# Performance work log

Measured on AMD Instinct MI355X. Metric: run time of the kernel, lower is better.

## Reference

```python
import jax, jax.numpy as jnp
import numpy as np
from jax import lax


def _dwconv1d(x, w, b):
    # x: (B, C, S); w: (C, 1, k) torch-style depthwise weight; pad (k-1)//2
    k = w.shape[-1]
    p = (k - 1) // 2
    y = lax.conv_general_dilated(
        x, w, window_strides=(1,), padding=[(p, p)],
        dimension_numbers=("NCH", "OIH", "NCH"),
        feature_group_count=x.shape[1])
    return y + b[None, :, None]


def setup_inputs() -> dict:
    key = jax.random.key(0)
    ks = jax.random.split(key, 8)
    B, S, D = 4, 8192, 768
    W = 3 * D
    s = 0.02
    return {
        "x": jax.random.normal(ks[0], (B, S, D), jnp.float32),
        "w_in": jax.random.normal(ks[1], (W, D), jnp.float32) * s,
        "b_in": jnp.zeros((W,), jnp.float32),
        "w_short": jax.random.normal(ks[2], (W, 1, 3), jnp.float32) * s,
        "b_short": jnp.zeros((W,), jnp.float32),
        "w_cond1": jax.random.normal(ks[3], (D, 1, 3), jnp.float32) * s,
        "b_cond1": jnp.zeros((D,), jnp.float32),
        "w_cond2": jax.random.normal(ks[4], (D, 1, 3), jnp.float32) * s,
        "b_cond2": jnp.zeros((D,), jnp.float32),
        "h0": jax.random.normal(ks[5], (1, S, D), jnp.float32) * s,
        "w_out": jax.random.normal(ks[6], (D, D), jnp.float32) * s,
        "b_out": jnp.zeros((D,), jnp.float32),
    }


def reference(x, w_in, b_in, w_short, b_short, w_cond1, b_cond1,
              w_cond2, b_cond2, h0, w_out, b_out):
    D = h0.shape[-1]
    # in projection: (B,S,3D)
    x3 = jnp.einsum("bsd,ed->bse", x, w_in) + b_in
    v = x3[..., 2 * D:]                       # (B,S,D)
    # conditioning branch: depthwise conv -> |rfft| -> depthwise conv
    v_t = jnp.swapaxes(v, 1, 2)               # (B,D,S)
    hc = _dwconv1d(v_t, w_cond1, b_cond1)     # (B,D,S)
    hmag = jnp.abs(jnp.fft.rfft(hc, axis=2))  # (B,D,E), E=S//2+1
    h_adapt_f = _dwconv1d(hmag, w_cond2, b_cond2)  # (B,D,E) real
    # short depthwise filter over all 3D channels
    x_t = jnp.swapaxes(x3, 1, 2)              # (B,3D,S)
    x_t = _dwconv1d(x_t, w_short, b_short)
    s1, s2, vv = jnp.split(x_t, 3, axis=1)    # each (B,D,S)
    y = vv * s1
    # adaptive long convolution in frequency domain
    h0_t = jnp.swapaxes(h0, 1, 2)             # (1,D,S)
    h0_f = jnp.fft.rfft(h0_t, axis=-1)        # (1,D,E) complex
    x_f = jnp.fft.rfft(y, axis=-1)            # (B,D,E) complex
    y = jnp.fft.irfft(x_f * (h0_f + h_adapt_f), axis=-1)  # (B,D,S)
    y = y * s2
    y = jnp.swapaxes(y, 1, 2)                 # (B,S,D)
    out = jnp.einsum("bsd,ed->bse", y, w_out) + b_out
    return out
```

## Files before the change

### kernel.cpp

```cpp
#include <hip/hip_runtime.h>
#include <math.h>


typedef unsigned short u16;
typedef short s16x8 __attribute__((ext_vector_type(8)));
typedef float f32x4 __attribute__((ext_vector_type(4)));
typedef u16 u16x8 __attribute__((ext_vector_type(8)));

#define LPZ(i) ((i) ^ (((i) >> 4) & 15) ^ (((i) >> 8) & 15))
#define BREV13(k) ((int)(__brev((unsigned)(k)) >> 19))
#define BREV12(k) ((int)(__brev((unsigned)(k)) >> 20))
#define CMUL(rr, ri, xr, xi, wr, wi) { rr = (xr)*(wr) - (xi)*(wi); ri = (xr)*(wi) + (xi)*(wr); }

__device__ __forceinline__ u16 f2bf(float f) {
  unsigned u = __float_as_uint(f);
  u = (u + 0x7FFFu + ((u >> 16) & 1u)) >> 16;
  return (u16)u;
}
__device__ __forceinline__ float bf2f(u16 u) { return __uint_as_float(((unsigned)u) << 16); }

__device__ __forceinline__ void glds16(const void* g, void* l) {
  __builtin_amdgcn_global_load_lds((const __attribute__((address_space(1))) unsigned*)g,
                                   (__attribute__((address_space(3))) unsigned*)l, 16, 0, 0);
}

__global__ __launch_bounds__(256) void cvt_bf16(const float* __restrict__ in,
                                                u16* __restrict__ out, int n8) {
  const int i = blockIdx.x * 256 + threadIdx.x;
  if (i < n8) {
    const float4 a = ((const float4*)in)[i * 2];
    const float4 b = ((const float4*)in)[i * 2 + 1];
    u16x8 r;
    r[0] = f2bf(a.x); r[1] = f2bf(a.y); r[2] = f2bf(a.z); r[3] = f2bf(a.w);
    r[4] = f2bf(b.x); r[5] = f2bf(b.y); r[6] = f2bf(b.z); r[7] = f2bf(b.w);
    ((u16x8*)out)[i] = r;
  }
}

template <int BIAS_M>
__global__ __launch_bounds__(256) void gemm_bt(const u16* __restrict__ A,
                                               const u16* __restrict__ B,
                                               const float* __restrict__ bias,
                                               void* __restrict__ Cout,
                                               int N, int K,
                                               size_t As_str, size_t Cs_str) {
  __shared__ __align__(16) u16 As[4096];
  __shared__ __align__(16) u16 Bs[4096];
  A += (size_t)blockIdx.z * As_str;
  const int tid = threadIdx.x;
  const int w = tid >> 6, l = tid & 63;
  const int m0 = blockIdx.y * 128, n0 = blockIdx.x * 128;
  const int wr = w >> 1, wc = w & 1;
  const int lr = l & 15, kc = l >> 4;

  const int p0 = w * 64 + l;
  const int p1 = p0 + 256;
  const int sl0 = (p0 & 7) ^ ((p0 >> 3) & 7);
  const int sl1 = (p1 & 7) ^ ((p1 >> 3) & 7);
  const int r0 = ((p0 >> 3) << 1) | (sl0 >> 2), ka = (sl0 & 3) << 3;
  const int r1 = ((p1 >> 3) << 1) | (sl1 >> 2), kb = (sl1 & 3) << 3;
  const u16* gA0 = A + (size_t)(m0 + r0) * K + ka;
  const u16* gA1 = A + (size_t)(m0 + r1) * K + kb;
  const u16* gB0 = B + (size_t)(n0 + r0) * K + ka;
  const u16* gB1 = B + (size_t)(n0 + r1) * K + kb;
  u16* lA0 = &As[(size_t)w * 512];
  u16* lA1 = &As[(size_t)(4 + w) * 512];
  u16* lB0 = &Bs[(size_t)w * 512];
  u16* lB1 = &Bs[(size_t)(4 + w) * 512];

  f32x4 acc[4][4] = {};

  for (int k0 = 0; k0 < K; k0 += 32) {
    glds16(gA0 + k0, lA0);
    glds16(gA1 + k0, lA1);
    glds16(gB0 + k0, lB0);
    glds16(gB1 + k0, lB1);
    __syncthreads();
    s16x8 af[4], bfr[4];
#pragma unroll
    for (int mi = 0; mi < 4; ++mi) {
      const int row = wr * 64 + mi * 16 + lr;
      const int slot = (((lr & 1) << 2) | kc) ^ ((lr >> 1) & 7);
      af[mi] = *(const s16x8*)&As[(row >> 1) * 64 + slot * 8];
    }
#pragma unroll
    for (int ni = 0; ni < 4; ++ni) {
      const int row = wc * 64 + ni * 16 + lr;
      const int slot = (((lr & 1) << 2) | kc) ^ ((lr >> 1) & 7);
      bfr[ni] = *(const s16x8*)&Bs[(row >> 1) * 64 + slot * 8];
    }
#pragma unroll
    for (int mi = 0; mi < 4; ++mi)
#pragma unroll
      for (int ni = 0; ni < 4; ++ni)
        acc[mi][ni] = __builtin_amdgcn_mfma_f32_16x16x32_bf16(af[mi], bfr[ni], acc[mi][ni], 0, 0, 0);
    __syncthreads();
  }

  const int rbase = m0 + wr * 64 + (kc << 2);
  const int cbase = n0 + wc * 64 + lr;
#pragma unroll
  for (int mi = 0; mi < 4; ++mi)
#pragma unroll
    for (int j = 0; j < 4; ++j) {
      const int row = rbase + mi * 16 + j;
      const float bm = BIAS_M ? bias[row] : 0.f;
#pragma unroll
      for (int ni = 0; ni < 4; ++ni) {
        const int col = cbase + ni * 16;
        const float v = acc[mi][ni][j] + (BIAS_M ? bm : bias[col]);
        if (BIAS_M) ((u16*)Cout)[(size_t)row * N + col] = f2bf(v);
        else ((float*)Cout)[(size_t)blockIdx.z * Cs_str + (size_t)row * N + col] = v;
      }
    }
}

__global__ void twfill(float2* __restrict__ tw) {
  const int k = blockIdx.x * 256 + threadIdx.x;
  if (k < 8192) {
    const double t = -2.0 * 3.14159265358979323846 * (double)k / 8192.0;
    tw[k] = make_float2((float)cos(t), (float)sin(t));
  }
}

__global__ __launch_bounds__(256) void transp(const float* __restrict__ in, float* __restrict__ out) {
  __shared__ float T[64][65];
  const int d0 = blockIdx.x * 64, s0 = blockIdx.y * 64;
  const int c = threadIdx.x & 63, r0 = threadIdx.x >> 6;
#pragma unroll
  for (int i = 0; i < 16; ++i) {
    const int r = r0 + i * 4;
    T[r][c] = in[(size_t)(s0 + r) * 768 + d0 + c];
  }
  __syncthreads();
#pragma unroll
  for (int i = 0; i < 16; ++i) {
    const int r = r0 + i * 4;
    out[(size_t)(d0 + r) * 8192 + s0 + c] = T[c][r];
  }
}

__device__ __forceinline__ void dif4(float2& A, float2& B, float2& C, float2& D,
                                     float2 w1, float2 w2, float2 w3) {
  const float apr = A.x + C.x, api = A.y + C.y, amr = A.x - C.x, ami = A.y - C.y;
  const float bpr = B.x + D.x, bpi = B.y + D.y, bmr = B.x - D.x, bmi = B.y - D.y;
  const float2 o0 = make_float2(apr + bpr, api + bpi);
  const float x1r = apr - bpr, x1i = api - bpi;
  float2 o1; CMUL(o1.x, o1.y, x1r, x1i, w2.x, w2.y);
  const float x2r = amr + bmi, x2i = ami - bmr;
  float2 o2; CMUL(o2.x, o2.y, x2r, x2i, w1.x, w1.y);
  const float x3r = amr - bmi, x3i = ami + bmr;
  float2 o3; CMUL(o3.x, o3.y, x3r, x3i, w3.x, w3.y);
  A = o0; B = o1; C = o2; D = o3;
}

__device__ __forceinline__ void dit4(float2& A, float2& B, float2& C, float2& D,
                                     float2 w1, float2 w2) {
  float vbr, vbi, vdr, vdi;
  CMUL(vbr, vbi, B.x, B.y, w2.x, w2.y);
  CMUL(vdr, vdi, D.x, D.y, w2.x, w2.y);
  const float a1r = A.x + vbr, a1i = A.y + vbi;
  const float b1r = A.x - vbr, b1i = A.y - vbi;
  const float c1r = C.x + vdr, c1i = C.y + vdi;
  const float d1r = C.x - vdr, d1i = C.y - vdi;
  float t1r, t1i, ur, ui;
  CMUL(t1r, t1i, c1r, c1i, w1.x, w1.y);
  CMUL(ur, ui, d1r, d1i, w1.y, -w1.x);
  A = make_float2(a1r + t1r, a1i + t1i);
  C = make_float2(a1r - t1r, a1i - t1i);
  B = make_float2(b1r + ur,  b1i + ui);
  D = make_float2(b1r - ur,  b1i - ui);
}

__device__ __forceinline__ void fwd_pass16(float2* z, const float2* __restrict__ tw,
                                           int base, int jp, int st, int e) {
  float2 v[16]; int idx[16];
#pragma unroll
  for (int m = 0; m < 16; ++m) { idx[m] = LPZ(base + m * st); v[m] = z[idx[m]]; }
#pragma unroll
  for (int c = 0; c < 4; ++c) {
    const int jc = jp + c * st;
    dif4(v[c], v[c + 4], v[c + 8], v[c + 12],
         tw[jc << e], tw[(2 * jc) << e], tw[(3 * jc) << e]);
  }
  const float2 u1 = tw[jp << (e + 2)];
  const float2 u2 = tw[(2 * jp) << (e + 2)];
  const float2 u3 = tw[(3 * jp) << (e + 2)];
#pragma unroll
  for (int a = 0; a < 4; ++a)
    dif4(v[4 * a], v[4 * a + 1], v[4 * a + 2], v[4 * a + 3], u1, u2, u3);
#pragma unroll
  for (int m = 0; m < 16; ++m) z[idx[m]] = v[m];
}

__device__ __forceinline__ void inv_pass16(float2* z, const float2* __restrict__ tw,
                                           int base, int jp, int st, int e) {
  float2 v[16]; int idx[16];
#pragma unroll
  for (int m = 0; m < 16; ++m) { idx[m] = LPZ(base + m * st); v[m] = z[idx[m]]; }
  const float2 w1 = tw[jp << e];
  const float2 w2 = tw[(2 * jp) << e];
#pragma unroll
  for (int a = 0; a < 4; ++a)
    dit4(v[4 * a], v[4 * a + 1], v[4 * a + 2], v[4 * a + 3], w1, w2);
#pragma unroll
  for (int c = 0; c < 4; ++c) {
    const int jpp = c * st + jp;
    dit4(v[c], v[c + 4], v[c + 8], v[c + 12],
         tw[jpp << (e - 2)], tw[(2 * jpp) << (e - 2)]);
  }
#pragma unroll
  for (int m = 0; m < 16; ++m) z[idx[m]] = v[m];
}

template <int NT>
__device__ __forceinline__ void fwd8192(float2* z, const float2* __restrict__ tw, int tid) {
  fwd_pass16(z, tw, tid, tid, 512, 0);
  __syncthreads();
  fwd_pass16(z, tw, ((tid >> 5) << 9) | (tid & 31), tid & 31, 32, 4);
  __syncthreads();
  fwd_pass16(z, tw, ((tid >> 1) << 5) | (tid & 1), tid & 1, 2, 8);
  __syncthreads();
#pragma unroll
  for (int t = 0; t < 8; ++t) {
    const int g = tid + t * 512;
    const int p = LPZ(2 * g), q = LPZ(2 * g + 1);
    const float2 U = z[p], V = z[q];
    z[p] = make_float2(U.x + V.x, U.y + V.y);
    z[q] = make_float2(U.x - V.x, U.y - V.y);
  }
  __syncthreads();
}

template <int NT>
__device__ __forceinline__ void inv4096(float2* z, const float2* __restrict__ tw, int tid) {
  if (tid < 256) inv_pass16(z, tw, tid << 4, 0, 1, 11);
  __syncthreads();
  if (tid < 256) inv_pass16(z, tw, ((tid >> 4) << 8) | (tid & 15), tid & 15, 16, 7);
  __syncthreads();
  if (tid < 256) inv_pass16(z, tw, tid, tid, 256, 3);
  __syncthreads();
}

__global__ __launch_bounds__(512, 2) void fft_h0_k(const float* __restrict__ h0T,
                                                   const float2* __restrict__ tw,
                                                   float2* __restrict__ h0f) {
  __shared__ float2 z[8192];
  const int d = blockIdx.x, tid = threadIdx.x;
  const float* src = h0T + (size_t)d * 8192;
  const int s0 = tid << 4;
#pragma unroll
  for (int m = 0; m < 16; ++m) z[LPZ(s0 + m)] = make_float2(src[s0 + m], 0.f);
  __syncthreads();
  fwd8192<512>(z, tw, tid);
  for (int k = tid; k <= 4096; k += 512) {
    h0f[(size_t)d * 4097 + k] = z[LPZ(BREV13(k))];
  }
}

__global__ __launch_bounds__(512, 2) void fused_fft(u16* __restrict__ x3T,
                                                    const float2* __restrict__ tw,
                                                    const float2* __restrict__ h0f,
                                                    const float* __restrict__ w_short,
                                                    const float* __restrict__ b_short,
                                                    const float* __restrict__ w_cond1,
                                                    const float* __restrict__ b_cond1,
                                                    const float* __restrict__ w_cond2,
                                                    const float* __restrict__ b_cond2,
                                                    size_t bstr) {
  __shared__ float2 z[8192];
  const int d = blockIdx.x, tid = threadIdx.x;
  x3T += (size_t)blockIdx.y * bstr;
  u16* g0 = x3T + (size_t)d * 8192;
  const u16* g1 = x3T + (size_t)(768 + d) * 8192;
  const u16* g2 = x3T + (size_t)(1536 + d) * 8192;

  const float q0 = w_cond1[d * 3], q1 = w_cond1[d * 3 + 1], q2 = w_cond1[d * 3 + 2], bc1 = b_cond1[d];
  const float t00 = w_short[d * 3], t01 = w_short[d * 3 + 1], t02 = w_short[d * 3 + 2], bs0 = b_short[d];
  const float t10 = w_short[(768 + d) * 3], t11 = w_short[(768 + d) * 3 + 1], t12 = w_short[(768 + d) * 3 + 2], bs1 = b_short[768 + d];
  const float t20 = w_short[(1536 + d) * 3], t21 = w_short[(1536 + d) * 3 + 1], t22 = w_short[(1536 + d) * 3 + 2], bs2 = b_short[1536 + d];

  const int s0 = tid << 4;

  {
    const u16x8 ga0 = *(const u16x8*)&g0[s0];
    const u16x8 ga1 = *(const u16x8*)&g0[s0 + 8];
    const u16x8 gb0 = *(const u16x8*)&g2[s0];
    const u16x8 gb1 = *(const u16x8*)&g2[s0 + 8];
    float a[18], bz[18];
    a[0]  = s0 ? bf2f(g0[s0 - 1]) : 0.f;
    bz[0] = s0 ? bf2f(g2[s0 - 1]) : 0.f;
#pragma unroll
    for (int m = 0; m < 8; ++m) {
      a[1 + m] = bf2f(ga0[m]);  a[9 + m] = bf2f(ga1[m]);
      bz[1 + m] = bf2f(gb0[m]); bz[9 + m] = bf2f(gb1[m]);
    }
    a[17]  = (s0 + 16 < 8192) ? bf2f(g0[s0 + 16]) : 0.f;
    bz[17] = (s0 + 16 < 8192) ? bf2f(g2[s0 + 16]) : 0.f;
#pragma unroll
    for (int m = 0; m < 16; ++m) {
      const float s1v = t00 * a[m] + t01 * a[m + 1] + t02 * a[m + 2] + bs0;
      const float vvv = t20 * bz[m] + t21 * bz[m + 1] + t22 * bz[m + 2] + bs2;
      const float hcv = q0 * bz[m] + q1 * bz[m + 1] + q2 * bz[m + 2] + bc1;
      z[LPZ(s0 + m)] = make_float2(hcv, s1v * vvv);
    }
  }
  __syncthreads();

  fwd8192<512>(z, tw, tid);

  float hm[9], yr[9], yi[9];
#pragma unroll
  for (int j = 0; j < 9; ++j) {
    const int k = tid + j * 512;
    if (k <= 4096) {
      const float2 Zk = z[LPZ(BREV13(k))];
      const float2 Zm = z[LPZ(BREV13((8192 - k) & 8191))];
      const float hcr = 0.5f * (Zk.x + Zm.x), hci = 0.5f * (Zk.y - Zm.y);
      hm[j] = sqrtf(hcr * hcr + hci * hci);
      yr[j] = 0.5f * (Zk.y + Zm.y);
      yi[j] = 0.5f * (Zm.x - Zk.x);
    }
  }
  __syncthreads();
  float* hbuf = (float*)z;
#pragma unroll
  for (int j = 0; j < 9; ++j) { const int k = tid + j * 512; if (k <= 4096) hbuf[k] = hm[j]; }
  __syncthreads();

  const float c0 = w_cond2[d * 3], c1 = w_cond2[d * 3 + 1], c2 = w_cond2[d * 3 + 2], bb2 = b_cond2[d];
  const float2* H0 = h0f + (size_t)d * 4097;
  float gr[9], gi[9];
#pragma unroll
  for (int j = 0; j < 9; ++j) {
    const int k = tid + j * 512;
    if (k <= 4096) {
      const float a = k ? hbuf[k - 1] : 0.f;
      const float m = hbuf[k];
      const float zn = (k < 4096) ? hbuf[k + 1] : 0.f;
      const float ha = c0 * a + c1 * m + c2 * zn + bb2;
      const float2 h = H0[k];
      const float hr = h.x + ha, hi = h.y;
      gr[j] = yr[j] * hr - yi[j] * hi;
      gi[j] = yr[j] * hi + yi[j] * hr;
      if (k == 0 || k == 4096) gi[j] = 0.f;
    }
  }
  __syncthreads();
#pragma unroll
  for (int j = 0; j < 9; ++j) {
    const int k = tid + j * 512;
    if (k <= 4096) z[LPZ(k)] = make_float2(gr[j], gi[j]);
  }
  __syncthreads();

  float zr2[8], zi2[8];
#pragma unroll
  for (int j = 0; j < 8; ++j) {
    const int kc = tid + j * 512;
    const float2 Ga = z[LPZ(kc)];
    const float2 Gb = z[LPZ(4096 - kc)];
    const float Er = 0.5f * (Ga.x + Gb.x), Ei = 0.5f * (Ga.y - Gb.y);
    const float Pr = 0.5f * (Ga.x - Gb.x), Pi = 0.5f * (Ga.y + Gb.y);
    const float2 w = tw[kc];
    const float Or = Pr * w.x + Pi * w.y;
    const float Oi = Pi * w.x - Pr * w.y;
    zr2[j] = Er - Oi;
    zi2[j] = -(Ei + Or);
  }
  __syncthreads();
#pragma unroll
  for (int j = 0; j < 8; ++j) {
    const int kc = tid + j * 512;
    z[LPZ(BREV12(kc))] = make_float2(zr2[j], zi2[j]);
  }
  __syncthreads();

  inv4096<512>(z, tw, tid);

  {
    const u16x8 g1a = *(const u16x8*)&g1[s0];
    const u16x8 g1b = *(const u16x8*)&g1[s0 + 8];
    float gg[18];
    gg[0] = s0 ? bf2f(g1[s0 - 1]) : 0.f;
#pragma unroll
    for (int m = 0; m < 8; ++m) { gg[1 + m] = bf2f(g1a[m]); gg[9 + m] = bf2f(g1b[m]); }
    gg[17] = (s0 + 16 < 8192) ? bf2f(g1[s0 + 16]) : 0.f;
    float2 zv[8];
#pragma unroll
    for (int r = 0; r < 8; ++r) zv[r] = z[LPZ((s0 >> 1) + r)];
    const float invM = 1.0f / 4096.0f;
    u16x8 o0, o1;
#pragma unroll
    for (int m = 0; m < 16; ++m) {
      const float xs = ((m & 1) ? -zv[m >> 1].y : zv[m >> 1].x) * invM;
      const float s2v = t10 * gg[m] + t11 * gg[m + 1] + t12 * gg[m + 2] + bs1;
      const u16 val = f2bf(xs * s2v);
      if (m < 8) o0[m] = val; else o1[m - 8] = val;
    }
    *(u16x8*)&g0[s0] = o0;
    *(u16x8*)&g0[s0 + 8] = o1;
  }
}

__global__ __launch_bounds__(256) void y2t(const u16* __restrict__ y2rows, u16* __restrict__ y2b,
                                           size_t in_str, size_t out_str) {
  __shared__ u16 T[64][65];
  y2rows += (size_t)blockIdx.z * in_str;
  y2b    += (size_t)blockIdx.z * out_str;
  const int d0 = blockIdx.x * 64, s0 = blockIdx.y * 64;
  const int c = threadIdx.x & 63, r0 = threadIdx.x >> 6;
#pragma unroll
  for (int i = 0; i < 16; ++i) {
    const int r = r0 + i * 4;
    T[r][c] = y2rows[(size_t)(d0 + r) * 8192 + s0 + c];
  }
  __syncthreads();
#pragma unroll
  for (int i = 0; i < 16; ++i) {
    const int r = r0 + i * 4;
    y2b[(size_t)(s0 + r) * 768 + d0 + c] = T[c][r];
  }
}

extern "C" void kernel_launch(void* const* d_in, const int* in_sizes, int n_in,
                              void* d_out, int out_size, void* d_ws, size_t ws_size,
                              hipStream_t stream) {
  (void)in_sizes; (void)n_in; (void)out_size;
  const float* x       = (const float*)d_in[0];
  const float* w_in    = (const float*)d_in[1];
  const float* b_in    = (const float*)d_in[2];
  const float* w_short = (const float*)d_in[3];
  const float* b_short = (const float*)d_in[4];
  const float* w_cond1 = (const float*)d_in[5];
  const float* b_cond1 = (const float*)d_in[6];
  const float* w_cond2 = (const float*)d_in[7];
  const float* b_cond2 = (const float*)d_in[8];
  const float* h0      = (const float*)d_in[9];
  const float* w_out   = (const float*)d_in[10];
  const float* b_out   = (const float*)d_in[11];

  float* ws = (float*)d_ws;
  float2* tw     = (float2*)ws;
  float2* h0f    = (float2*)(ws + 16384);
  u16*    xb     = (u16*)(ws + 6309376);
  u16*    w_inb  = (u16*)(ws + 9455104);
  u16*    w_outb = (u16*)(ws + 10339840);
  u16*    x3Tb   = (u16*)(ws + 10634752);
  float*  h0T    = (float*)(ws + 6309376);

  const size_t BSTR = 18874368ull;
  const bool merged = ws_size >= 193533952ull;

  twfill<<<32, 256, 0, stream>>>(tw);
  transp<<<dim3(12, 128), 256, 0, stream>>>(h0, h0T);
  fft_h0_k<<<768, 512, 0, stream>>>(h0T, tw, h0f);
  cvt_bf16<<<864, 256, 0, stream>>>(w_in, w_inb, 221184);
  cvt_bf16<<<288, 256, 0, stream>>>(w_out, w_outb, 73728);

  if (merged) {
    for (int b = 0; b < 4; ++b) {
      cvt_bf16<<<3072, 256, 0, stream>>>(x + (size_t)b * 6291456, xb, 786432);
      gemm_bt<1><<<dim3(64, 18), 256, 0, stream>>>(w_inb, xb, b_in,
                                                   x3Tb + (size_t)b * BSTR, 8192, 768, 0, 0);
    }
    fused_fft<<<dim3(768, 4), 512, 0, stream>>>(x3Tb, tw, h0f,
                                                w_short, b_short, w_cond1, b_cond1,
                                                w_cond2, b_cond2, BSTR);
    y2t<<<dim3(12, 128, 4), 256, 0, stream>>>(x3Tb, x3Tb + 6291456, BSTR, BSTR);
    gemm_bt<0><<<dim3(6, 64, 4), 256, 0, stream>>>(x3Tb + 6291456, w_outb, b_out,
                                                   (float*)d_out, 768, 768,
                                                   BSTR, 6291456ull);
  } else {
    for (int b = 0; b < 4; ++b) {
      cvt_bf16<<<3072, 256, 0, stream>>>(x + (size_t)b * 6291456, xb, 786432);
      gemm_bt<1><<<dim3(64, 18), 256, 0, stream>>>(w_inb, xb, b_in, x3Tb, 8192, 768, 0, 0);
      fused_fft<<<dim3(768, 1), 512, 0, stream>>>(x3Tb, tw, h0f,
                                                  w_short, b_short, w_cond1, b_cond1,
                                                  w_cond2, b_cond2, 0);
      y2t<<<dim3(12, 128, 1), 256, 0, stream>>>(x3Tb, x3Tb + 6291456, 0, 0);
      gemm_bt<0><<<dim3(6, 64, 1), 256, 0, stream>>>(x3Tb + 6291456, w_outb, b_out,
                                                     (float*)d_out + (size_t)b * 6291456,
                                                     768, 768, 0, 0);
    }
  }
}
```

Baseline: 579.4 us.

## Batch input GEMM over all batches and pair h0 FFTs via complex packing

Adds a workspace tier that converts all of x to bf16 at once and runs the input projection GEMM as a single batched launch over the z grid dimension, instead of four serial convert+GEMM launches. The GEMM gains a B-operand batch stride and a batched output stride for the bf16 path. The h0 filter FFT now packs two real channels into one complex transform and separates them with conjugate symmetry, halving the number of FFT blocks. The new batched path needs a larger workspace, and it only runs when the workspace passes that larger size threshold.

```diff
diff --git a/kernel.cpp b/kernel.cpp
--- a/kernel.cpp
+++ b/kernel.cpp
@@ -43,10 +43,11 @@
                                                const float* __restrict__ bias,
                                                void* __restrict__ Cout,
                                                int N, int K,
-                                               size_t As_str, size_t Cs_str) {
+                                               size_t As_str, size_t Bs_str, size_t Cs_str) {
   __shared__ __align__(16) u16 As[4096];
   __shared__ __align__(16) u16 Bs[4096];
   A += (size_t)blockIdx.z * As_str;
+  B += (size_t)blockIdx.z * Bs_str;
   const int tid = threadIdx.x;
   const int w = tid >> 6, l = tid & 63;
   const int m0 = blockIdx.y * 128, n0 = blockIdx.x * 128;
@@ -109,7 +110,7 @@
       for (int ni = 0; ni < 4; ++ni) {
         const int col = cbase + ni * 16;
         const float v = acc[mi][ni][j] + (BIAS_M ? bm : bias[col]);
-        if (BIAS_M) ((u16*)Cout)[(size_t)row * N + col] = f2bf(v);
+        if (BIAS_M) ((u16*)Cout)[(size_t)blockIdx.z * Cs_str + (size_t)row * N + col] = f2bf(v);
         else ((float*)Cout)[(size_t)blockIdx.z * Cs_str + (size_t)row * N + col] = v;
       }
     }
@@ -242,19 +243,25 @@
   __syncthreads();
 }
 
-__global__ __launch_bounds__(512, 2) void fft_h0_k(const float* __restrict__ h0T,
-                                                   const float2* __restrict__ tw,
-                                                   float2* __restrict__ h0f) {
+__global__ __launch_bounds__(512, 2) void fft_h0_pair(const float* __restrict__ h0T,
+                                                      const float2* __restrict__ tw,
+                                                      float2* __restrict__ h0f) {
   __shared__ float2 z[8192];
-  const int d = blockIdx.x, tid = threadIdx.x;
-  const float* src = h0T + (size_t)d * 8192;
+  const int d0 = blockIdx.x * 2, tid = threadIdx.x;
+  const float* srcA = h0T + (size_t)d0 * 8192;
+  const float* srcB = srcA + 8192;
   const int s0 = tid << 4;
 #pragma unroll
-  for (int m = 0; m < 16; ++m) z[LPZ(s0 + m)] = make_float2(src[s0 + m], 0.f);
+  for (int m = 0; m < 16; ++m) z[LPZ(s0 + m)] = make_float2(srcA[s0 + m], srcB[s0 + m]);
   __syncthreads();
   fwd8192<512>(z, tw, tid);
+  float2* H0 = h0f + (size_t)d0 * 4097;
+  float2* H1 = H0 + 4097;
   for (int k = tid; k <= 4096; k += 512) {
-    h0f[(size_t)d * 4097 + k] = z[LPZ(BREV13(k))];
+    const float2 Zk = z[LPZ(BREV13(k))];
+    const float2 Zm = z[LPZ(BREV13((8192 - k) & 8191))];
+    H0[k] = make_float2(0.5f * (Zk.x + Zm.x), 0.5f * (Zk.y - Zm.y));
+    H1[k] = make_float2(0.5f * (Zk.y + Zm.y), 0.5f * (Zm.x - Zk.x));
   }
 }
 
@@ -441,47 +448,72 @@
   const float* b_out   = (const float*)d_in[11];
 
   float* ws = (float*)d_ws;
-  float2* tw     = (float2*)ws;
-  float2* h0f    = (float2*)(ws + 16384);
-  u16*    xb     = (u16*)(ws + 6309376);
-  u16*    w_inb  = (u16*)(ws + 9455104);
-  u16*    w_outb = (u16*)(ws + 10339840);
-  u16*    x3Tb   = (u16*)(ws + 10634752);
-  float*  h0T    = (float*)(ws + 6309376);
-
+  float2* tw  = (float2*)ws;
+  float2* h0f = (float2*)(ws + 16384);
+  float*  h0T = ws + 6309376;
   const size_t BSTR = 18874368ull;
-  const bool merged = ws_size >= 193533952ull;
+  const size_t XSTR = 6291456ull;
+
+  const bool t1 = ws_size >= 231282688ull;
+  const bool t2 = !t1 && ws_size >= 193533952ull;
 
   twfill<<<32, 256, 0, stream>>>(tw);
   transp<<<dim3(12, 128), 256, 0, stream>>>(h0, h0T);
-  fft_h0_k<<<768, 512, 0, stream>>>(h0T, tw, h0f);
-  cvt_bf16<<<864, 256, 0, stream>>>(w_in, w_inb, 221184);
-  cvt_bf16<<<288, 256, 0, stream>>>(w_out, w_outb, 73728);
-
-  if (merged) {
+  fft_h0_pair<<<384, 512, 0, stream>>>(h0T, tw, h0f);
+
+  if (t1) {
+    u16* xb4    = (u16*)(ws + 6309376);
+    u16* w_inb  = (u16*)(ws + 18892288);
+    u16* w_outb = (u16*)(ws + 19777024);
+    u16* x3Tb4  = (u16*)(ws + 20071936);
+    cvt_bf16<<<864, 256, 0, stream>>>(w_in, w_inb, 221184);
+    cvt_bf16<<<288, 256, 0, stream>>>(w_out, w_outb, 73728);
+    cvt_bf16<<<12288, 256, 0, stream>>>(x, xb4, 3145728);
+    gemm_bt<1><<<dim3(64, 18, 4), 256, 0, stream>>>(w_inb, xb4, b_in, x3Tb4,
+                                                    8192, 768, 0, XSTR, BSTR);
+    fused_fft<<<dim3(768, 4), 512, 0, stream>>>(x3Tb4, tw, h0f,
+                                                w_short, b_short, w_cond1, b_cond1,
+                                                w_cond2, b_cond2, BSTR);
+    y2t<<<dim3(12, 128, 4), 256, 0, stream>>>(x3Tb4, x3Tb4 + XSTR, BSTR, BSTR);
+    gemm_bt<0><<<dim3(6, 64, 4), 256, 0, stream>>>(x3Tb4 + XSTR, w_outb, b_out,
+                                                   (float*)d_out, 768, 768,
+                                                   BSTR, 0, XSTR);
+  } else if (t2) {
+    u16* xb     = (u16*)(ws + 6309376);
+    u16* w_inb  = (u16*)(ws + 9455104);
+    u16* w_outb = (u16*)(ws + 10339840);
+    u16* x3Tb   = (u16*)(ws + 10634752);
+    cvt_bf16<<<864, 256, 0, stream>>>(w_in, w_inb, 221184);
+    cvt_bf16<<<288, 256, 0, stream>>>(w_out, w_outb, 73728);
     for (int b = 0; b < 4; ++b) {
-      cvt_bf16<<<3072, 256, 0, stream>>>(x + (size_t)b * 6291456, xb, 786432);
+      cvt_bf16<<<3072, 256, 0, stream>>>(x + (size_t)b * XSTR, xb, 786432);
       gemm_bt<1><<<dim3(64, 18), 256, 0, stream>>>(w_inb, xb, b_in,
-                                                   x3Tb + (size_t)b * BSTR, 8192, 768, 0, 0);
+                                                   x3Tb + (size_t)b * BSTR, 8192, 768, 0, 0, 0);
     }
     fused_fft<<<dim3(768, 4), 512, 0, stream>>>(x3Tb, tw, h0f,
                                                 w_short, b_short, w_cond1, b_cond1,
                                                 w_cond2, b_cond2, BSTR);
-    y2t<<<dim3(12, 128, 4), 256, 0, stream>>>(x3Tb, x3Tb + 6291456, BSTR, BSTR);
-    gemm_bt<0><<<dim3(6, 64, 4), 256, 0, stream>>>(x3Tb + 6291456, w_outb, b_out,
+    y2t<<<dim3(12, 128, 4), 256, 0, stream>>>(x3Tb, x3Tb + XSTR, BSTR, BSTR);
+    gemm_bt<0><<<dim3(6, 64, 4), 256, 0, stream>>>(x3Tb + XSTR, w_outb, b_out,
                                                    (float*)d_out, 768, 768,
-                                                   BSTR, 6291456ull);
+                                                   BSTR, 0, XSTR);
   } else {
+    u16* xb     = (u16*)(ws + 6309376);
+    u16* w_inb  = (u16*)(ws + 9455104);
+    u16* w_outb = (u16*)(ws + 10339840);
+    u16* x3Tb   = (u16*)(ws + 10634752);
+    cvt_bf16<<<864, 256, 0, stream>>>(w_in, w_inb, 221184);
+    cvt_bf16<<<288, 256, 0, stream>>>(w_out, w_outb, 73728);
     for (int b = 0; b < 4; ++b) {
-      cvt_bf16<<<3072, 256, 0, stream>>>(x + (size_t)b * 6291456, xb, 786432);
-      gemm_bt<1><<<dim3(64, 18), 256, 0, stream>>>(w_inb, xb, b_in, x3Tb, 8192, 768, 0, 0);
+      cvt_bf16<<<3072, 256, 0, stream>>>(x + (size_t)b * XSTR, xb, 786432);
+      gemm_bt<1><<<dim3(64, 18), 256, 0, stream>>>(w_inb, xb, b_in, x3Tb, 8192, 768, 0, 0, 0);
       fused_fft<<<dim3(768, 1), 512, 0, stream>>>(x3Tb, tw, h0f,
                                                   w_short, b_short, w_cond1, b_cond1,
                                                   w_cond2, b_cond2, 0);
-      y2t<<<dim3(12, 128, 1), 256, 0, stream>>>(x3Tb, x3Tb + 6291456, 0, 0);
-      gemm_bt<0><<<dim3(6, 64, 1), 256, 0, stream>>>(x3Tb + 6291456, w_outb, b_out,
-                                                     (float*)d_out + (size_t)b * 6291456,
-                                                     768, 768, 0, 0);
-    }
-  }
-}
+      y2t<<<dim3(12, 128, 1), 256, 0, stream>>>(x3Tb, x3Tb + XSTR, 0, 0);
+      gemm_bt<0><<<dim3(6, 64, 1), 256, 0, stream>>>(x3Tb + XSTR, w_outb, b_out,
+                                                     (float*)d_out + (size_t)b * XSTR,
+                                                     768, 768, 0, 0, 0);
+    }
+  }
+}
```

After: 535.2 us. 1.08x faster.
